# Kernel tuning notes

Measured on AMD Instinct MI355X. Metric: run time of the kernel, lower is better.

The kernel has to match this reference:

```python
import jax, jax.numpy as jnp
import numpy as np

B = 256          # graphs per batch
NPG = 512        # nodes per graph (equal-size AIGs)
N = B * NPG      # 131072 total nodes
E = 2 * N        # AIG: ~2 fanins per AND node
H = 256          # hidden_channels
EMB = 3          # node-type embedding dim
IN = EMB + 1     # node_encoder_out_channels


def _p(k, shape, fan_in):
    return jax.random.normal(k, shape, jnp.float32) / np.float32(np.sqrt(fan_in))


def setup_inputs():
    key = jax.random.key(0)
    ks = list(jax.random.split(key, 24))
    nt = jax.random.randint(ks[0], (N, 1), 0, 3)
    ninv = jax.random.randint(ks[1], (N, 1), 0, 3)
    x = jnp.concatenate([nt, ninv], axis=1).astype(jnp.int32)
    # within-graph random edges
    epg = E // B
    gid = jnp.repeat(jnp.arange(B), epg)
    src = gid * NPG + jax.random.randint(ks[2], (E,), 0, NPG)
    dst = gid * NPG + jax.random.randint(ks[3], (E,), 0, NPG)
    edge_index = jnp.stack([src, dst]).astype(jnp.int32)
    batch = jnp.repeat(jnp.arange(B), NPG).astype(jnp.int32)
    d = dict(x=x, edge_index=edge_index, batch=batch)
    d['emb_w'] = _p(ks[4], (3, EMB), 1)
    d['c1_lW'] = _p(ks[5], (IN, H), IN); d['c1_lb'] = jnp.zeros((H,), jnp.float32)
    d['c1_rW'] = _p(ks[6], (IN, H), IN)
    d['t1'] = jnp.float32(0.1)
    d['c2_lW'] = _p(ks[7], (H, H), H); d['c2_lb'] = jnp.zeros((H,), jnp.float32)
    d['c2_rW'] = _p(ks[8], (H, H), H)
    d['t2'] = jnp.float32(0.1)
    d['mlp_W'] = _p(ks[9], (NPG * H, H), NPG * H); d['mlp_b'] = jnp.zeros((H,), jnp.float32)
    d['gru_Wih'] = _p(ks[10], (3 * H, H), H); d['gru_Whh'] = _p(ks[11], (3 * H, H), H)
    d['gru_bih'] = jnp.zeros((3 * H,), jnp.float32); d['gru_bhh'] = jnp.zeros((3 * H,), jnp.float32)
    d['st_Wq'] = _p(ks[12], (3, H, H), H); d['st_bq'] = jnp.zeros((3, H), jnp.float32)
    d['st_Wk'] = _p(ks[13], (3, H, H), H); d['st_bk'] = jnp.zeros((3, H), jnp.float32)
    d['st_Wv'] = _p(ks[14], (3, H, H), H); d['st_bv'] = jnp.zeros((3, H), jnp.float32)
    d['st_Wo'] = _p(ks[15], (3, H, H), H); d['st_bo'] = jnp.zeros((3, H), jnp.float32)
    d['st_lW'] = _p(ks[16], (3, H, H), H); d['st_lb'] = jnp.zeros((3, H), jnp.float32)
    d['pma_lW'] = _p(ks[17], (H, H), H); d['pma_lb'] = jnp.zeros((H,), jnp.float32)
    d['seed'] = _p(ks[18], (1, H), H)
    d['fin_W'] = _p(ks[19], (3 * H, 3 * H), 3 * H); d['fin_b'] = jnp.zeros((3 * H,), jnp.float32)
    return d


def _softmax_aggr(msg, idx, t, n):
    # PyG SoftmaxAggregation: alpha = softmax(msg * t per target segment); sum(msg * alpha)
    logits = msg * t                                   # [E, C]
    m = jax.ops.segment_max(logits, idx, num_segments=n)
    m = jnp.where(jnp.isfinite(m), m, 0.0)             # empty segments -> 0
    ex = jnp.exp(logits - m[idx])
    s = jax.ops.segment_sum(ex, idx, num_segments=n)
    alpha = ex / s[idx]
    return jax.ops.segment_sum(msg * alpha, idx, num_segments=n)


def _sage(h, edge_index, lW, lb, rW, t):
    # SAGEConv: lin_l(softmax_aggr(x_j -> i)) + lin_r(x_i)
    msg = h[edge_index[0]]                             # gather sources [E, C]
    ag = _softmax_aggr(msg, edge_index[1], t, N)       # scatter-softmax-scatter
    return ag @ lW + lb + h @ rW


def _gru_last(xd, Wih, Whh, bih, bhh):
    # torch GRU over [B, T, H]; return last output
    def step(h, x_t):
        gi = x_t @ Wih.T + bih
        gh = h @ Whh.T + bhh
        ir, iz, inn = jnp.split(gi, 3, axis=-1)
        hr, hz, hn = jnp.split(gh, 3, axis=-1)
        r = jax.nn.sigmoid(ir + hr)
        z = jax.nn.sigmoid(iz + hz)
        nn_ = jnp.tanh(inn + r * hn)
        h_new = (1.0 - z) * nn_ + z * h
        return h_new, None
    h0 = jnp.zeros((xd.shape[0], H), xd.dtype)
    hT, _ = jax.lax.scan(step, h0, jnp.swapaxes(xd, 0, 1))
    return hT


def _mab(q, k, Wq, bq, Wk, bk, Wv, bv, Wo, bo, Wl, bl):
    # Set-Transformer MAB, 1 head, no layer norm (PyG defaults)
    Q = q @ Wq + bq
    K = k @ Wk + bk
    V = k @ Wv + bv
    A = jax.nn.softmax(jnp.einsum('bqd,bkd->bqk', Q, K) / np.float32(np.sqrt(H)), axis=-1)
    h = q + (jnp.einsum('bqk,bkd->bqd', A, V) @ Wo + bo)
    return h + jax.nn.relu(h @ Wl + bl)


def _set_transformer(xd, Wq, bq, Wk, bk, Wv, bv, Wo, bo, Wl, bl, pma_lW, pma_lb, seed):
    def mab_i(i, q, k):
        return _mab(q, k, Wq[i], bq[i], Wk[i], bk[i], Wv[i], bv[i], Wo[i], bo[i], Wl[i], bl[i])
    h = mab_i(0, xd, xd)                               # encoder SAB [B, NPG, H]
    kk = jax.nn.relu(h @ pma_lW + pma_lb)
    s = jnp.broadcast_to(seed[None], (xd.shape[0], 1, H))
    s = mab_i(1, s, kk)                                # PMA (1 seed)
    s = mab_i(2, s, s)                                 # decoder SAB
    return s.reshape(xd.shape[0], H)


def _forward(x, edge_index, batch, emb_w, c1_lW, c1_lb, c1_rW, t1, c2_lW, c2_lb, c2_rW, t2,
             mlp_W, mlp_b, gru_Wih, gru_Whh, gru_bih, gru_bhh,
             st_Wq, st_bq, st_Wk, st_bk, st_Wv, st_bv, st_Wo, st_bo, st_lW, st_lb,
             pma_lW, pma_lb, seed, fin_W, fin_b):
    # NodeEncoder: embed node_type, concat num_inverted_predecessors as float
    h = jnp.concatenate([emb_w[x[:, 0]], x[:, 1:2].astype(jnp.float32)], axis=1)  # [N, 4]
    h = jax.nn.relu(_sage(h, edge_index, c1_lW, c1_lb, c1_rW, t1))
    h = jax.nn.relu(_sage(h, edge_index, c2_lW, c2_lb, c2_rW, t2))
    # equal-size sorted graphs -> dense batch is a reshape
    xd = h.reshape(B, NPG, H)
    p1 = xd.reshape(B, NPG * H) @ mlp_W + mlp_b                       # MLPAggregation
    p2 = _gru_last(xd, gru_Wih, gru_Whh, gru_bih, gru_bhh)            # GRUAggregation
    p3 = _set_transformer(xd, st_Wq, st_bq, st_Wk, st_bk, st_Wv, st_bv,
                          st_Wo, st_bo, st_lW, st_lb, pma_lW, pma_lb, seed)
    pooled = jnp.concatenate([p1, p2, p3], axis=1)                    # [B, 3H]
    return pooled @ fin_W + fin_b


def reference(x, edge_index, batch, emb_w, c1_lW, c1_lb, c1_rW, t1, c2_lW, c2_lb, c2_rW, t2,
              mlp_W, mlp_b, gru_Wih, gru_Whh, gru_bih, gru_bhh,
              st_Wq, st_bq, st_Wk, st_bk, st_Wv, st_bv, st_Wo, st_bo, st_lW, st_lb,
              pma_lW, pma_lb, seed, fin_W, fin_b):
    return _forward(x, edge_index, batch, emb_w, c1_lW, c1_lb, c1_rW, t1, c2_lW, c2_lb, c2_rW, t2,
                    mlp_W, mlp_b, gru_Wih, gru_Whh, gru_bih, gru_bhh,
                    st_Wq, st_bq, st_Wk, st_bk, st_Wv, st_bv, st_Wo, st_bo, st_lW, st_lb,
                    pma_lW, pma_lb, seed, fin_W, fin_b)
```

## Files before the change

kernel.cpp:

```cpp
#include <hip/hip_runtime.h>
#include <hip/hip_bf16.h>
#include <math.h>

constexpr int NN   = 131072;
constexpr int NE   = 262144;
constexpr int BG   = 256;

typedef __bf16 bf16x8 __attribute__((ext_vector_type(8)));
typedef float  f32x4  __attribute__((ext_vector_type(4)));
typedef int    i32x4  __attribute__((ext_vector_type(4)));

__device__ inline float sigm(float x){ return 1.f/(1.f+__expf(-x)); }
__device__ inline float blo(unsigned u){ union{unsigned a;float f;}v; v.a=u<<16; return v.f; }
__device__ inline float bhi(unsigned u){ union{unsigned a;float f;}v; v.a=u&0xffff0000u; return v.f; }
__device__ inline float b2f(ushort u){ union{unsigned a;float f;}v; v.a=((unsigned)u)<<16; return v.f; }
__device__ inline unsigned short f2bu(float f){
  union{float f;unsigned u;}v; v.f=f;
  unsigned u = v.u + 0x7fffu + ((v.u>>16)&1u);
  return (unsigned short)(u>>16);
}
__device__ inline bf16x8 cvt8(float4 a, float4 b){
  union { ushort u[8]; bf16x8 v; } r;
  r.u[0]=f2bu(a.x); r.u[1]=f2bu(a.y); r.u[2]=f2bu(a.z); r.u[3]=f2bu(a.w);
  r.u[4]=f2bu(b.x); r.u[5]=f2bu(b.y); r.u[6]=f2bu(b.z); r.u[7]=f2bu(b.w);
  return r.v;
}

__global__ void k_zero(int* __restrict__ p, int n){
  int i = blockIdx.x*256 + threadIdx.x;
  if (i < n) p[i] = 0;
}

__global__ void k_node_enc(const int* __restrict__ x, const float* __restrict__ emb,
                           float* __restrict__ h0){
  int n = blockIdx.x*256 + threadIdx.x;
  if (n >= NN) return;
  int nt = x[2*n], ninv = x[2*n+1];
  float4 v; v.x = emb[nt*3+0]; v.y = emb[nt*3+1]; v.z = emb[nt*3+2]; v.w = (float)ninv;
  reinterpret_cast<float4*>(h0)[n] = v;
}

__global__ void k_count(const int* __restrict__ ei, int* __restrict__ deg){
  int e = blockIdx.x*256 + threadIdx.x;
  if (e >= NE) return;
  atomicAdd(&deg[ei[NE + e]], 1);
}
__global__ void k_blocksum(const int* __restrict__ deg, int* __restrict__ bsum){
  __shared__ int sd[256];
  int t = threadIdx.x;
  const int* p = deg + blockIdx.x*1024;
  int s = p[t*4] + p[t*4+1] + p[t*4+2] + p[t*4+3];
  sd[t]=s; __syncthreads();
  for (int d=128; d>0; d>>=1){ if (t<d) sd[t]+=sd[t+d]; __syncthreads(); }
  if (!t) bsum[blockIdx.x] = sd[0];
}
__global__ void k_scanbsum(const int* __restrict__ bsum, int* __restrict__ boff, int* __restrict__ offN){
  __shared__ int s[128];
  int t = threadIdx.x;
  int mine = bsum[t];
  s[t]=mine; __syncthreads();
  for (int d=1; d<128; d<<=1){ int v = (t>=d)? s[t-d]:0; __syncthreads(); s[t]+=v; __syncthreads(); }
  boff[t] = s[t]-mine;
  if (t==127) offN[0] = s[127];
}
__global__ void k_scanchunk(const int* __restrict__ deg, const int* __restrict__ boff, int* __restrict__ offs){
  __shared__ int ts[256];
  int t = threadIdx.x, b = blockIdx.x;
  const int* p = deg + b*1024;
  int v0=p[t*4],v1=p[t*4+1],v2=p[t*4+2],v3=p[t*4+3];
  int mysum=v0+v1+v2+v3;
  ts[t]=mysum; __syncthreads();
  for (int d=1; d<256; d<<=1){ int v=(t>=d)?ts[t-d]:0; __syncthreads(); ts[t]+=v; __syncthreads(); }
  int ex = ts[t]-mysum + boff[b];
  int* o = offs + b*1024 + t*4;
  o[0]=ex; o[1]=ex+v0; o[2]=ex+v0+v1; o[3]=ex+v0+v1+v2;
}
__global__ void k_fill(const int* __restrict__ ei, const int* __restrict__ offs,
                       int* __restrict__ cur, int* __restrict__ esrc){
  int e = blockIdx.x*256 + threadIdx.x;
  if (e >= NE) return;
  int dst = ei[NE+e];
  int pos = offs[dst] + atomicAdd(&cur[dst],1);
  esrc[pos] = ei[e];
}

__global__ void k_aggr4(const float* __restrict__ h, const int* __restrict__ offs,
                        const int* __restrict__ esrc, const float* __restrict__ tptr,
                        float* __restrict__ ag){
  int n = blockIdx.x*256 + threadIdx.x;
  if (n >= NN) return;
  int s = offs[n], e = offs[n+1];
  float4 z = {0,0,0,0};
  if (s == e){ reinterpret_cast<float4*>(ag)[n] = z; return; }
  float t = *tptr;
  float4 num=z, den=z;
  for (int i=s;i<e;++i){
    float4 v = reinterpret_cast<const float4*>(h)[esrc[i]];
    float ex;
    ex=__expf(v.x*t); num.x+=v.x*ex; den.x+=ex;
    ex=__expf(v.y*t); num.y+=v.y*ex; den.y+=ex;
    ex=__expf(v.z*t); num.z+=v.z*ex; den.z+=ex;
    ex=__expf(v.w*t); num.w+=v.w*ex; den.w+=ex;
  }
  float4 r = {num.x/den.x, num.y/den.y, num.z/den.z, num.w/den.w};
  reinterpret_cast<float4*>(ag)[n] = r;
}

__global__ __launch_bounds__(256) void k_aggr256(float* __restrict__ buf, const int* __restrict__ offs,
                          const int* __restrict__ esrc, const float* __restrict__ tptr, int base){
  int n = base + blockIdx.x, c = threadIdx.x;
  int s = offs[n], e = offs[n+1];
  float* outp = buf + (size_t)blockIdx.x*512 + 256 + c;
  if (s == e){ *outp = 0.f; return; }
  float t = *tptr;
  float num=0.f, den=0.f;
  for (int i=s;i<e;++i){
    float v = buf[(size_t)(esrc[i]-base)*512 + c];
    float ex = __expf(v*t);
    num += v*ex; den += ex;
  }
  *outp = num/den;
}

__global__ __launch_bounds__(256) void k_conv1_lin(const float* __restrict__ ag, const float* __restrict__ h0,
                            const float* __restrict__ lW, const float* __restrict__ lb,
                            const float* __restrict__ rW, float* __restrict__ out, int base){
  int n = base + blockIdx.x, c = threadIdx.x;
  float4 a  = reinterpret_cast<const float4*>(ag)[n];
  float4 xv = reinterpret_cast<const float4*>(h0)[n];
  float acc = lb[c];
  acc += a.x*lW[c]  + a.y*lW[256+c]  + a.z*lW[512+c]  + a.w*lW[768+c];
  acc += xv.x*rW[c] + xv.y*rW[256+c] + xv.z*rW[512+c] + xv.w*rW[768+c];
  out[(size_t)blockIdx.x*512 + c] = fmaxf(acc, 0.f);
}

#define GF_BIAS    1
#define GF_RELU    2
#define GF_RESID   4
#define GF_RESID_B 8
#define GF_ADDC    32
#define GF_ATOMIC  64
#define GF_BF16    128
#define GF_VTP     256
#define GF_RESID16 512

__global__ void k_packb(const float* __restrict__ W, ushort* __restrict__ Bp, int K, int N){
  int idx = blockIdx.x*256 + threadIdx.x;
  if (idx >= K*N) return;
  int k = idx / N, j = idx - k*N;
  Bp[((size_t)(k>>3)*N + j)*8 + (k&7)] = f2bu(W[idx]);
}
__global__ void k_packbT(const float* __restrict__ W, ushort* __restrict__ Bp, int K, int N){
  int idx = blockIdx.x*256 + threadIdx.x;
  if (idx >= K*N) return;
  int j = idx / K, k = idx - j*K;
  Bp[((size_t)(k>>3)*N + j)*8 + (k&7)] = f2bu(W[idx]);
}
__global__ __launch_bounds__(256) void k_packhh8(const float* __restrict__ gWhh,
                        char* __restrict__ Bp8, float* __restrict__ cs){
  int j = blockIdx.x, k = threadIdx.x;
  float w = gWhh[(size_t)j*256 + k];
  __shared__ float red[256];
  red[k] = fabsf(w); __syncthreads();
  for (int d=128; d>0; d>>=1){ if (k<d) red[k]=fmaxf(red[k],red[k+d]); __syncthreads(); }
  float mx = fmaxf(red[0], 1e-20f);
  int q = (int)lrintf(w * (127.f/mx));
  q = max(-127, min(127, q));
  Bp8[((size_t)(k>>3)*768 + j)*8 + (k&7)] = (char)q;
  if (k==0) cs[j] = mx/(127.f*127.f);
}
__global__ void k_packbias(const float* __restrict__ gbih, const float* __restrict__ gbhh,
                           float* __restrict__ bc){
  int i = blockIdx.x*256 + threadIdx.x;
  if (i >= 1024) return;
  int c = i & 255;
  float v;
  if (i < 256)      v = gbih[c] + gbhh[c];
  else if (i < 512) v = gbih[256+c] + gbhh[256+c];
  else if (i < 768) v = gbih[512+c];
  else              v = gbhh[512+c];
  bc[i] = v;
}

template<int FLAGS>
__global__ __launch_bounds__(256) void k_bgemm(const float* __restrict__ A, const ushort* __restrict__ Bp,
                       const float* __restrict__ bias, const float* __restrict__ resid,
                       float* __restrict__ C, int M, int Nn, int K, int lda){
  const int tid = threadIdx.x;
  const int wv = tid>>6, lane = tid&63;
  const int mw = wv>>1, nw = wv&1;
  const int arow = lane&15, ks = lane>>4;
  const int m0 = blockIdx.x*128 + mw*64, n0 = blockIdx.y*128 + nw*64;
  f32x4 acc[4][4] = {};
  #pragma unroll 2
  for (int k0 = 0; k0 < K; k0 += 32){
    const int kb = (k0>>3) + ks;
    bf16x8 af[4];
    #pragma unroll
    for (int mf=0; mf<4; ++mf){
      const float4* p = reinterpret_cast<const float4*>(A + (size_t)(m0+mf*16+arow)*lda + k0 + ks*8);
      af[mf] = cvt8(p[0], p[1]);
    }
    #pragma unroll
    for (int nf=0; nf<4; ++nf){
      const int col = n0 + nf*16 + arow;
      bf16x8 bfr = *reinterpret_cast<const bf16x8*>(Bp + ((size_t)kb*Nn + col)*8);
      #pragma unroll
      for (int mf=0; mf<4; ++mf)
        acc[mf][nf] = __builtin_amdgcn_mfma_f32_16x16x32_bf16(af[mf], bfr, acc[mf][nf], 0, 0, 0);
    }
  }
  #pragma unroll
  for (int nf=0; nf<4; ++nf){
    const int n = n0 + nf*16 + arow;
    float bv  = (FLAGS & GF_BIAS)    ? bias[n]  : 0.f;
    float rbv = (FLAGS & GF_RESID_B) ? resid[n] : 0.f;
    #pragma unroll
    for (int mf=0; mf<4; ++mf){
      #pragma unroll
      for (int r=0; r<4; ++r){
        const int m = m0 + mf*16 + ks*4 + r;
        size_t idx = (size_t)m*Nn + n;
        float v = acc[mf][nf][r];
        v += bv;
        if (FLAGS & GF_RELU)  v = fmaxf(v, 0.f);
        if (FLAGS & GF_RESID) v += resid[idx];
        v += rbv;
        C[idx] = v;
      }
    }
  }
}

template<int FLAGS, bool ABF>
__global__ __launch_bounds__(256) void k_bgemm2(const void* __restrict__ Av, const ushort* __restrict__ Bp,
                       const float* __restrict__ bias, const void* __restrict__ residv,
                       void* __restrict__ Cv, int K, int lda){
  const int tid = threadIdx.x;
  const int wv = tid>>6, lane = tid&63;
  const int mw = wv&1, nw = wv>>1;
  const int arow = lane&15, ks = lane>>4;
  const int m0 = blockIdx.x*128 + mw*64;
  const int n0 = nw*128;
  const int kChunk = K / gridDim.z, kBeg = blockIdx.z * kChunk;
  f32x4 acc[4][8] = {};
  #pragma unroll 1
  for (int k0 = kBeg; k0 < kBeg+kChunk; k0 += 32){
    const int kb = (k0>>3) + ks;
    bf16x8 af[4];
    if (ABF){
      const ushort* A = (const ushort*)Av;
      #pragma unroll
      for (int mf=0; mf<4; ++mf)
        af[mf] = *reinterpret_cast<const bf16x8*>(A + (size_t)(m0+mf*16+arow)*lda + k0 + ks*8);
    } else {
      const float* A = (const float*)Av;
      #pragma unroll
      for (int mf=0; mf<4; ++mf){
        const float4* p = reinterpret_cast<const float4*>(A + (size_t)(m0+mf*16+arow)*lda + k0 + ks*8);
        af[mf] = cvt8(p[0], p[1]);
      }
    }
    #pragma unroll
    for (int nf=0; nf<8; ++nf){
      const int col = n0 + nf*16 + arow;
      bf16x8 bfr = *reinterpret_cast<const bf16x8*>(Bp + ((size_t)kb*256 + col)*8);
      #pragma unroll
      for (int mf=0; mf<4; ++mf)
        acc[mf][nf] = __builtin_amdgcn_mfma_f32_16x16x32_bf16(af[mf], bfr, acc[mf][nf], 0, 0, 0);
    }
  }
  #pragma unroll
  for (int nf=0; nf<8; ++nf){
    const int n = n0 + nf*16 + arow;
    float bv = (FLAGS & GF_BIAS) ? bias[n] : 0.f;
    #pragma unroll
    for (int mf=0; mf<4; ++mf){
      #pragma unroll
      for (int r=0; r<4; ++r){
        const int m = m0 + mf*16 + ks*4 + r;
        size_t idx = (size_t)m*256 + n;
        float v = acc[mf][nf][r];
        if (FLAGS & GF_ATOMIC){ atomicAdd((float*)Cv + idx, v); }
        else {
          v += bv;
          if (FLAGS & GF_RELU) v = fmaxf(v, 0.f);
          if (FLAGS & GF_RESID16) v += b2f(((const ushort*)residv)[idx]);
          if (FLAGS & GF_VTP){
            const int rr = m & 511, mg = m >> 9;
            ((ushort*)Cv)[(size_t)mg*131072 + (((rr>>3)*256 + n)<<3) + (rr&7)] = f2bu(v);
          } else if (FLAGS & GF_BF16){
            ((ushort*)Cv)[idx] = f2bu(v);
          } else {
            ((float*)Cv)[idx] = v;
          }
        }
      }
    }
  }
}

__global__ __launch_bounds__(256) void k_qk16(const ushort* __restrict__ Qb, const ushort* __restrict__ Kb,
                                              float* __restrict__ S){
  const int tid = threadIdx.x;
  const int wv = tid>>6, lane = tid&63;
  const int mw = wv>>1, nw = wv&1;
  const int arow = lane&15, ks = lane>>4;
  const int m0 = blockIdx.x*128 + mw*64;
  const int n0 = blockIdx.y*128 + nw*64;
  const int g  = blockIdx.x>>2;
  const ushort* Kg = Kb + (size_t)g*131072;
  f32x4 acc[4][4] = {};
  #pragma unroll
  for (int k0 = 0; k0 < 256; k0 += 32){
    bf16x8 af[4];
    #pragma unroll
    for (int mf=0; mf<4; ++mf)
      af[mf] = *reinterpret_cast<const bf16x8*>(Qb + (size_t)(m0+mf*16+arow)*256 + k0 + ks*8);
    #pragma unroll
    for (int nf=0; nf<4; ++nf){
      const int j = n0 + nf*16 + arow;
      bf16x8 bfr = *reinterpret_cast<const bf16x8*>(Kg + (size_t)j*256 + k0 + ks*8);
      #pragma unroll
      for (int mf=0; mf<4; ++mf)
        acc[mf][nf] = __builtin_amdgcn_mfma_f32_16x16x32_bf16(af[mf], bfr, acc[mf][nf], 0, 0, 0);
    }
  }
  #pragma unroll
  for (int nf=0; nf<4; ++nf){
    const int n = n0 + nf*16 + arow;
    #pragma unroll
    for (int mf=0; mf<4; ++mf){
      #pragma unroll
      for (int r=0; r<4; ++r){
        const int m = m0 + mf*16 + ks*4 + r;
        S[(size_t)m*512 + n] = acc[mf][nf][r];
      }
    }
  }
}

__global__ __launch_bounds__(256) void k_smrow(const float* __restrict__ S, ushort* __restrict__ P){
  const int row = blockIdx.x, tid = threadIdx.x;
  __shared__ float red[4];
  const float* sr = S + (size_t)row*512;
  float s0 = sr[tid], s1 = sr[tid+256];
  float m = fmaxf(s0, s1);
  #pragma unroll
  for (int o=1;o<64;o<<=1) m = fmaxf(m, __shfl_xor(m,o));
  if ((tid&63)==0) red[tid>>6] = m;
  __syncthreads();
  m = fmaxf(fmaxf(red[0],red[1]), fmaxf(red[2],red[3]));
  __syncthreads();
  float e0 = __expf((s0-m)*0.0625f), e1 = __expf((s1-m)*0.0625f);
  float s = e0+e1;
  #pragma unroll
  for (int o=1;o<64;o<<=1) s += __shfl_xor(s,o);
  if ((tid&63)==0) red[tid>>6] = s;
  __syncthreads();
  s = red[0]+red[1]+red[2]+red[3];
  float inv = 1.f/s;
  P[(size_t)row*512 + tid]       = f2bu(e0*inv);
  P[(size_t)row*512 + 256 + tid] = f2bu(e1*inv);
}

__global__ __launch_bounds__(256) void k_av2(const ushort* __restrict__ Pb, const ushort* __restrict__ VTp,
                                             ushort* __restrict__ Ob){
  const int tid = threadIdx.x;
  const int wv = tid>>6, lane = tid&63;
  const int mw = wv&1, nw = wv>>1;
  const int arow = lane&15, ks = lane>>4;
  const int m0 = blockIdx.x*128 + mw*64;
  const int n0 = nw*128;
  const int g  = blockIdx.x>>2;
  const ushort* Vg = VTp + (size_t)g*131072;
  f32x4 acc[4][8] = {};
  #pragma unroll 1
  for (int k0 = 0; k0 < 512; k0 += 32){
    const int kb = (k0>>3) + ks;
    bf16x8 af[4];
    #pragma unroll
    for (int mf=0; mf<4; ++mf)
      af[mf] = *reinterpret_cast<const bf16x8*>(Pb + (size_t)(m0+mf*16+arow)*512 + k0 + ks*8);
    #pragma unroll
    for (int nf=0; nf<8; ++nf){
      const int col = n0 + nf*16 + arow;
      bf16x8 bfr = *reinterpret_cast<const bf16x8*>(Vg + ((size_t)kb*256 + col)*8);
      #pragma unroll
      for (int mf=0; mf<4; ++mf)
        acc[mf][nf] = __builtin_amdgcn_mfma_f32_16x16x32_bf16(af[mf], bfr, acc[mf][nf], 0, 0, 0);
    }
  }
  #pragma unroll
  for (int nf=0; nf<8; ++nf){
    const int n = n0 + nf*16 + arow;
    #pragma unroll
    for (int mf=0; mf<4; ++mf){
      #pragma unroll
      for (int r=0; r<4; ++r){
        const int m = m0 + mf*16 + ks*4 + r;
        Ob[(size_t)m*256 + n] = f2bu(acc[mf][nf][r]);
      }
    }
  }
}

__global__ void k_rowbias(const float* __restrict__ bias, float* __restrict__ C, int Nn, int total){
  int i = blockIdx.x*256 + threadIdx.x;
  if (i < total) C[i] = bias[i % Nn];
}
__global__ void k_qvec(const float* __restrict__ seed, const float* __restrict__ Wq,
                       const float* __restrict__ bq, float* __restrict__ qv){
  __shared__ float s[256];
  int t = threadIdx.x;
  s[t] = seed[t]; __syncthreads();
  float acc = bq[t];
  for (int c = 0; c < 256; ++c) acc += s[c] * Wq[c*256 + t];
  qv[t] = acc;
}
__global__ __launch_bounds__(256) void k_wk2q(const float* __restrict__ Wk2, const float* __restrict__ bk2,
                      const float* __restrict__ qv, float* __restrict__ outv){
  __shared__ float qs[256];
  __shared__ float red[4];
  int t = threadIdx.x;
  qs[t] = qv[t]; __syncthreads();
  float a = 0.f;
  for (int c=0;c<256;c+=4){
    float4 w = *reinterpret_cast<const float4*>(Wk2 + t*256 + c);
    a += w.x*qs[c] + w.y*qs[c+1] + w.z*qs[c+2] + w.w*qs[c+3];
  }
  outv[t] = a;
  float bb = bk2[t]*qs[t];
  #pragma unroll
  for (int o=1;o<64;o<<=1) bb += __shfl_xor(bb,o);
  if ((t&63)==0) red[t>>6] = bb;
  __syncthreads();
  if (t==0) outv[256] = red[0]+red[1]+red[2]+red[3];
}
__global__ __launch_bounds__(256) void k_pmafuse16(const ushort* __restrict__ kkb, const float* __restrict__ wkq,
                        float* __restrict__ wsum){
  int g = blockIdx.x, tid = threadIdx.x;
  __shared__ float qs[256];
  __shared__ float sc[512];
  __shared__ float red[4];
  qs[tid] = wkq[tid];
  __syncthreads();
  const float b2q = wkq[256];
  const ushort* kg = kkb + (size_t)g*512*256;
  float l0=0.f, l1=0.f;
  for (int j0=0;j0<2;++j0){
    int j = tid + j0*256;
    const ushort* kr = kg + (size_t)j*256;
    float a = 0.f;
    for (int c8=0;c8<32;++c8){
      uint4 kv = *reinterpret_cast<const uint4*>(kr + c8*8);
      const float* qq = qs + c8*8;
      a += qq[0]*blo(kv.x)+qq[1]*bhi(kv.x)+qq[2]*blo(kv.y)+qq[3]*bhi(kv.y)
         + qq[4]*blo(kv.z)+qq[5]*bhi(kv.z)+qq[6]*blo(kv.w)+qq[7]*bhi(kv.w);
    }
    a = (a + b2q)*0.0625f;
    if (j0) l1=a; else l0=a;
  }
  float m = fmaxf(l0,l1);
  #pragma unroll
  for (int o=1;o<64;o<<=1) m = fmaxf(m, __shfl_xor(m,o));
  if ((tid&63)==0) red[tid>>6] = m;
  __syncthreads();
  m = fmaxf(fmaxf(red[0],red[1]), fmaxf(red[2],red[3]));
  __syncthreads();
  float e0 = __expf(l0-m), e1 = __expf(l1-m);
  sc[tid]=e0; sc[tid+256]=e1;
  float s = e0+e1;
  #pragma unroll
  for (int o=1;o<64;o<<=1) s += __shfl_xor(s,o);
  if ((tid&63)==0) red[tid>>6] = s;
  __syncthreads();
  s = red[0]+red[1]+red[2]+red[3];
  float invs = 1.f/s;
  float acc = 0.f;
  for (int j=0;j<512;++j) acc += sc[j] * b2f(kg[(size_t)j*256 + tid]);
  wsum[(size_t)g*256+tid] = acc*invs;
}
__global__ void k_concat(const float* __restrict__ p1, const float* __restrict__ p2,
                         const float* __restrict__ p3, float* __restrict__ pooled){
  int idx = blockIdx.x*256 + threadIdx.x;
  int b = idx / 768, j = idx % 768;
  float v = (j < 256) ? p1[b*256+j] : (j < 512) ? p2[b*256+j-256] : p3[b*256+j-512];
  pooled[idx] = v;
}

__global__ __launch_bounds__(512) void k_gru12(const ushort* __restrict__ X,
                      const ushort* __restrict__ pIh, const char* __restrict__ pHh8,
                      const float* __restrict__ csg, const float* __restrict__ bc,
                      float* __restrict__ p2){
  extern __shared__ char gsm[];
  float*  GIw  = (float*)gsm;
  float*  gh   = (float*)(gsm + 98304);
  float*  bcl  = (float*)(gsm + 101376);
  float*  csl  = (float*)(gsm + 105472);
  char*   hbf8 = (char*) (gsm + 108544);
  const int g = blockIdx.x;
  const int tid = threadIdx.x;
  const int wv = tid>>6, lane = tid&63;
  const int arow = lane&15, ks = lane>>4;
  for (int i=tid;i<1024;i+=512) bcl[i] = bc[i];
  for (int i=tid;i<768;i+=512)  csl[i] = csg[i];
  if (tid < 256) hbf8[tid] = 0;
  float h_reg = 0.f;
  const ushort* Xg = X + (size_t)g*512*256;
  __syncthreads();
  for (int w=0; w<16; ++w){
    const int t0 = w*32;
    #pragma unroll
    for (int mt=0; mt<2; ++mt){
      const ushort* xr = Xg + (size_t)(t0 + mt*16 + arow)*256;
      f32x4 acc[6] = {};
      #pragma unroll
      for (int kt=0; kt<8; ++kt){
        bf16x8 af = *reinterpret_cast<const bf16x8*>(xr + kt*32 + ks*8);
        #pragma unroll
        for (int nt=0; nt<6; ++nt){
          bf16x8 bfr = *reinterpret_cast<const bf16x8*>(pIh + ((size_t)(kt*4+ks)*768 + wv*96+nt*16+arow)*8);
          acc[nt] = __builtin_amdgcn_mfma_f32_16x16x32_bf16(af, bfr, acc[nt], 0,0,0);
        }
      }
      #pragma unroll
      for (int nt=0; nt<6; ++nt){
        const int col = wv*96 + nt*16 + arow;
        #pragma unroll
        for (int r=0;r<4;++r)
          GIw[(size_t)(mt*16 + ks*4 + r)*768 + col] = acc[nt][r];
      }
    }
    for (int dt=0; dt<32; ++dt){
      i32x4 sacc[6] = {};
      #pragma unroll
      for (int kt=0; kt<8; ++kt){
        long a8 = 0;
        if (arow == 0) a8 = *reinterpret_cast<const long*>(hbf8 + kt*32 + ks*8);
        #pragma unroll
        for (int nt=0; nt<6; ++nt){
          const int col = wv*96 + nt*16 + arow;
          long b8 = *reinterpret_cast<const long*>(pHh8 + ((size_t)(kt*4+ks)*768 + col)*8);
          sacc[nt] = __builtin_amdgcn_mfma_i32_16x16x32_i8(a8, b8, sacc[nt], 0,0,0);
        }
      }
      if (ks == 0){
        #pragma unroll
        for (int nt=0; nt<6; ++nt){
          const int col = wv*96 + nt*16 + arow;
          gh[col] = (float)sacc[nt][0] * csl[col];
        }
      }
      __syncthreads();
      if (tid < 256){
        const int c = tid;
        const float* gir = GIw + (size_t)dt*768;
        float rr = sigm(gir[c]     + gh[c]     + bcl[c]);
        float zz = sigm(gir[256+c] + gh[256+c] + bcl[256+c]);
        float nx = gir[512+c] + bcl[512+c] + rr*(gh[512+c] + bcl[768+c]);
        nx = fminf(fmaxf(nx, -15.f), 15.f);
        float e2 = __expf(2.f*nx);
        float nn = (e2-1.f)*__builtin_amdgcn_rcpf(e2+1.f);
        h_reg = (1.f-zz)*nn + zz*h_reg;
        int q = (int)lrintf(h_reg*127.f);
        q = max(-127, min(127, q));
        hbf8[c] = (char)q;
      }
      __syncthreads();
    }
  }
  if (tid < 256) p2[(size_t)g*256 + tid] = h_reg;
}

extern "C" void kernel_launch(void* const* d_in, const int* in_sizes, int n_in,
                              void* d_out, int out_size, void* d_ws, size_t ws_size,
                              hipStream_t stream){
  const int*   x      = (const int*)  d_in[0];
  const int*   ei     = (const int*)  d_in[1];
  const float* emb_w  = (const float*)d_in[3];
  const float* c1_lW  = (const float*)d_in[4];
  const float* c1_lb  = (const float*)d_in[5];
  const float* c1_rW  = (const float*)d_in[6];
  const float* t1     = (const float*)d_in[7];
  const float* c2_lW  = (const float*)d_in[8];
  const float* c2_lb  = (const float*)d_in[9];
  const float* c2_rW  = (const float*)d_in[10];
  const float* t2     = (const float*)d_in[11];
  const float* mlp_W  = (const float*)d_in[12];
  const float* mlp_b  = (const float*)d_in[13];
  const float* gWih   = (const float*)d_in[14];
  const float* gWhh   = (const float*)d_in[15];
  const float* gbih   = (const float*)d_in[16];
  const float* gbhh   = (const float*)d_in[17];
  const float* stWq   = (const float*)d_in[18];
  const float* stbq   = (const float*)d_in[19];
  const float* stWk   = (const float*)d_in[20];
  const float* stbk   = (const float*)d_in[21];
  const float* stWv   = (const float*)d_in[22];
  const float* stbv   = (const float*)d_in[23];
  const float* stWo   = (const float*)d_in[24];
  const float* stbo   = (const float*)d_in[25];
  const float* stlW   = (const float*)d_in[26];
  const float* stlb   = (const float*)d_in[27];
  const float* pma_lW = (const float*)d_in[28];
  const float* pma_lb = (const float*)d_in[29];
  const float* seed   = (const float*)d_in[30];
  const float* fin_W  = (const float*)d_in[31];
  const float* fin_b  = (const float*)d_in[32];
  float* out = (float*)d_out;

  auto needFor = [](int CHe)->size_t{
    size_t bufN = (size_t)CHe*512*512;
    size_t floats = (size_t)33554432 + 3*bufN + 2*524288 + 2*196608 + 8*65536 + 196608 + 320 + 512;
    size_t ints   = 131072 + 131200 + 131072 + 262144 + 128 + 128;
    return floats*4 + ints*4 + 4096;
  };
  const int CHe = (ws_size >= needFor(64)) ? 64 : 32;
  if (ws_size < needFor(32)) return;
  const int NCHUNKe = BG / CHe;
  const int NCNe = CHe * 512;
  const size_t bufN = (size_t)CHe*512*512;

  float* H2   = (float*)d_ws;
  float* bufA = H2   + (size_t)33554432;
  float* bufB = bufA + bufN;
  float* bufC = bufB + bufN;
  float* h0   = bufC + bufN;
  float* ag1  = h0   + (size_t)524288;
  float* wT1  = ag1  + (size_t)524288;
  float* wT2  = wT1  + (size_t)196608;
  float* p1   = wT2  + (size_t)196608;
  float* p2   = p1   + (size_t)65536;
  float* p3   = p2   + (size_t)65536;
  float* av2  = p3   + (size_t)65536;
  float* s1   = av2  + (size_t)65536;
  float* s2v  = s1   + (size_t)65536;
  float* v3   = s2v  + (size_t)65536;
  float* h3   = v3   + (size_t)65536;
  float* pooled = h3 + (size_t)65536;
  float* qv   = pooled + (size_t)196608;
  int*   deg  = (int*)(qv + 320);
  int*   offs = deg  + 131072;
  int*   cur  = offs + 131200;
  int*   esrc = cur  + 131072;
  int*   bsum = esrc + 262144;
  int*   boff = bsum + 128;
  float* wkq  = (float*)(boff + 128);

  ushort* H2b  = (ushort*)H2;
  ushort* pIh  = (ushort*)wT1;
  char*   pHh8 = (char*)(wT1 + 98304);
  float*  csHh = wT1 + 98304 + 49152;
  ushort* pC2  = (ushort*)wT2;
  float*  bcomb= wT2 + 65536;
  float*  pa   = h0;
  ushort* pQ0  = (ushort*)(pa);
  ushort* pK0  = (ushort*)(pa + 32768);
  ushort* pV0  = (ushort*)(pa + 65536);
  ushort* pO0  = (ushort*)(pa + 98304);
  ushort* pL0  = (ushort*)(pa + 131072);
  ushort* pPma = (ushort*)(pa + 163840);
  ushort* pV1  = (ushort*)(pa + 229376);
  ushort* pO1  = (ushort*)(pa + 262144);
  ushort* pL1  = (ushort*)(pa + 294912);
  ushort* pV2  = (ushort*)(pa + 327680);
  ushort* pO2  = (ushort*)(pa + 360448);
  ushort* pL2  = (ushort*)(pa + 393216);
  ushort* pFin = (ushort*)(pa + 425984);

  ushort* Qbf = (ushort*)bufA;
  ushort* Obf = (ushort*)(bufA + bufN/4);
  ushort* VTp = (ushort*)(bufA + bufN/2);
  ushort* Kbf = (ushort*)bufB;
  ushort* Pbf = (ushort*)(bufB + bufN/4);
  ushort* Ebf = Qbf;
  ushort* kkb = Kbf;

  const int ls0 = 65536, ls1 = 256;

  k_node_enc<<<NN/256, 256, 0, stream>>>(x, emb_w, h0);

  k_zero<<<NN/256, 256, 0, stream>>>(deg, NN);
  k_count<<<NE/256, 256, 0, stream>>>(ei, deg);
  k_blocksum<<<128, 256, 0, stream>>>(deg, bsum);
  k_scanbsum<<<1, 128, 0, stream>>>(bsum, boff, offs + NN);
  k_scanchunk<<<128, 256, 0, stream>>>(deg, boff, offs);
  k_zero<<<NN/256, 256, 0, stream>>>(cur, NN);
  k_fill<<<NE/256, 256, 0, stream>>>(ei, offs, cur, esrc);

  k_aggr4<<<NN/256, 256, 0, stream>>>(h0, offs, esrc, t1, ag1);
  k_packb <<<256, 256, 0, stream>>>(c2_rW, pC2, 256, 256);
  k_packb <<<256, 256, 0, stream>>>(c2_lW, pC2 + 65536, 256, 256);
  k_packbT<<<768, 256, 0, stream>>>(gWih, pIh, 256, 768);
  k_packhh8<<<768, 256, 0, stream>>>(gWhh, pHh8, csHh);
  k_packbias<<<4, 256, 0, stream>>>(gbih, gbhh, bcomb);

  for (int cg = 0; cg < NCHUNKe; ++cg){
    const int base = cg * NCNe;
    ushort* Hcb = H2b + (size_t)base * 256;
    k_conv1_lin<<<NCNe, 256, 0, stream>>>(ag1, h0, c1_lW, c1_lb, c1_rW, bufA, base);
    k_aggr256<<<NCNe, 256, 0, stream>>>(bufA, offs, esrc, t2, base);
    k_bgemm2<GF_BIAS|GF_RELU|GF_BF16, false><<<NCNe/128, 256, 0, stream>>>(bufA, pC2, c2_lb, nullptr, Hcb, 512, 512);
  }

  k_packb<<<131072, 256, 0, stream>>>(mlp_W, (ushort*)bufB, 131072, 256);
  k_rowbias<<<256, 256, 0, stream>>>(mlp_b, p1, 256, 65536);
  k_bgemm2<GF_ATOMIC, true><<<dim3(2, 1, 128), 256, 0, stream>>>(H2b, (ushort*)bufB, nullptr, nullptr, p1, NN, 131072);

  k_gru12<<<BG, 512, 108800, stream>>>(H2b, pIh, pHh8, csHh, bcomb, p2);

  k_packb<<<256, 256, 0, stream>>>(stWq,        pQ0, 256, 256);
  k_packb<<<256, 256, 0, stream>>>(stWk,        pK0, 256, 256);
  k_packb<<<256, 256, 0, stream>>>(stWv,        pV0, 256, 256);
  k_packb<<<256, 256, 0, stream>>>(stWo,        pO0, 256, 256);
  k_packb<<<256, 256, 0, stream>>>(stlW,        pL0, 256, 256);
  k_packb<<<256, 256, 0, stream>>>(pma_lW,      pPma,256, 256);
  k_packb<<<256, 256, 0, stream>>>(stWv + ls0,  pV1, 256, 256);
  k_packb<<<256, 256, 0, stream>>>(stWo + ls0,  pO1, 256, 256);
  k_packb<<<256, 256, 0, stream>>>(stlW + ls0,  pL1, 256, 256);
  k_packb<<<256, 256, 0, stream>>>(stWv + 2*ls0,pV2, 256, 256);
  k_packb<<<256, 256, 0, stream>>>(stWo + 2*ls0,pO2, 256, 256);
  k_packb<<<256, 256, 0, stream>>>(stlW + 2*ls0,pL2, 256, 256);
  k_packb<<<2304, 256, 0, stream>>>(fin_W,      pFin,768, 768);
  k_qvec<<<1, 256, 0, stream>>>(seed, stWq + ls0, stbq + ls1, qv);
  k_wk2q<<<1, 256, 0, stream>>>(stWk + ls0, stbk + ls1, qv, wkq);

  for (int cg = 0; cg < NCHUNKe; ++cg){
    const int base = cg * NCNe;
    ushort* Hcb = H2b + (size_t)base * 256;
    const int gb1 = NCNe/128;
    k_bgemm2<GF_BIAS|GF_BF16, true><<<gb1, 256, 0, stream>>>(Hcb, pQ0, stbq, nullptr, Qbf, 256, 256);
    k_bgemm2<GF_BIAS|GF_BF16, true><<<gb1, 256, 0, stream>>>(Hcb, pK0, stbk, nullptr, Kbf, 256, 256);
    k_bgemm2<GF_BIAS|GF_VTP,  true><<<gb1, 256, 0, stream>>>(Hcb, pV0, stbv, nullptr, VTp, 256, 256);
    k_qk16<<<dim3(gb1, 4), 256, 0, stream>>>(Qbf, Kbf, bufC);
    k_smrow<<<NCNe, 256, 0, stream>>>(bufC, Pbf);
    k_av2<<<gb1, 256, 0, stream>>>(Pbf, VTp, Obf);
    k_bgemm2<GF_BIAS|GF_RESID16|GF_BF16, true><<<gb1, 256, 0, stream>>>(Obf, pO0, stbo, Hcb, Hcb, 256, 256);
    k_bgemm2<GF_BIAS|GF_RELU|GF_RESID16|GF_BF16, true><<<gb1, 256, 0, stream>>>(Hcb, pL0, stlb, Hcb, Ebf, 256, 256);
    k_bgemm2<GF_BIAS|GF_RELU|GF_BF16, true><<<gb1, 256, 0, stream>>>(Ebf, pPma, pma_lb, nullptr, kkb, 256, 256);
    k_pmafuse16<<<CHe, 256, 0, stream>>>(kkb, wkq, av2 + (size_t)cg*CHe*256);
  }

  k_bgemm<GF_BIAS><<<dim3(2, 2, 1), 256, 0, stream>>>(av2, pV1, stbv + ls1, nullptr, v3, 256, 256, 256, 256);
  k_bgemm<GF_BIAS|GF_RESID_B><<<dim3(2, 2, 1), 256, 0, stream>>>(v3, pO1, stbo + ls1, seed, s1, 256, 256, 256, 256);
  k_bgemm<GF_BIAS|GF_RELU|GF_RESID><<<dim3(2, 2, 1), 256, 0, stream>>>(s1, pL1, stlb + ls1, s1, s2v, 256, 256, 256, 256);
  k_bgemm<GF_BIAS><<<dim3(2, 2, 1), 256, 0, stream>>>(s2v, pV2, stbv + 2*ls1, nullptr, v3, 256, 256, 256, 256);
  k_bgemm<GF_BIAS|GF_RESID><<<dim3(2, 2, 1), 256, 0, stream>>>(v3, pO2, stbo + 2*ls1, s2v, h3, 256, 256, 256, 256);
  k_bgemm<GF_BIAS|GF_RELU|GF_RESID><<<dim3(2, 2, 1), 256, 0, stream>>>(h3, pL2, stlb + 2*ls1, h3, p3, 256, 256, 256, 256);

  k_concat<<<768, 256, 0, stream>>>(p1, p2, p3, pooled);
  k_bgemm<GF_BIAS><<<dim3(2, 6, 1), 256, 0, stream>>>(pooled, pFin, fin_b, nullptr, out, 256, 768, 768, 768);
}
```

Baseline: 2.732 ms.

## Fuse QK, softmax and AV into one LDS-resident attention kernel; bf16 conv2 staging

Replaces the three-kernel attention (QK^T to global fp32 scores, row softmax, then P·V) with one kernel per 64-row tile. The score tile stays in 132KB of LDS, is softmaxed in place, and is converted to bf16 on the fly for the AV MFMA, with normalisation applied at the output. This removes the global round trip of the 512x512 fp32 score matrix and the bf16 P matrix. Separately, the conv1 output and conv2 aggregation buffer are now stored as bf16, so the GEMM reads bf16 directly and memory traffic is lower, at some precision cost. The large LDS footprint limits each CU to one block.

```diff
diff --git a/kernel.cpp b/kernel.cpp
--- a/kernel.cpp
+++ b/kernel.cpp
@@ -106,32 +106,32 @@
   reinterpret_cast<float4*>(ag)[n] = r;
 }
 
-__global__ __launch_bounds__(256) void k_aggr256(float* __restrict__ buf, const int* __restrict__ offs,
+__global__ __launch_bounds__(256) void k_aggr256(ushort* __restrict__ buf, const int* __restrict__ offs,
                           const int* __restrict__ esrc, const float* __restrict__ tptr, int base){
   int n = base + blockIdx.x, c = threadIdx.x;
   int s = offs[n], e = offs[n+1];
-  float* outp = buf + (size_t)blockIdx.x*512 + 256 + c;
-  if (s == e){ *outp = 0.f; return; }
+  ushort* outp = buf + (size_t)blockIdx.x*512 + 256 + c;
+  if (s == e){ *outp = 0; return; }
   float t = *tptr;
   float num=0.f, den=0.f;
   for (int i=s;i<e;++i){
-    float v = buf[(size_t)(esrc[i]-base)*512 + c];
+    float v = b2f(buf[(size_t)(esrc[i]-base)*512 + c]);
     float ex = __expf(v*t);
     num += v*ex; den += ex;
   }
-  *outp = num/den;
+  *outp = f2bu(num/den);
 }
 
 __global__ __launch_bounds__(256) void k_conv1_lin(const float* __restrict__ ag, const float* __restrict__ h0,
                             const float* __restrict__ lW, const float* __restrict__ lb,
-                            const float* __restrict__ rW, float* __restrict__ out, int base){
+                            const float* __restrict__ rW, ushort* __restrict__ out, int base){
   int n = base + blockIdx.x, c = threadIdx.x;
   float4 a  = reinterpret_cast<const float4*>(ag)[n];
   float4 xv = reinterpret_cast<const float4*>(h0)[n];
   float acc = lb[c];
   acc += a.x*lW[c]  + a.y*lW[256+c]  + a.z*lW[512+c]  + a.w*lW[768+c];
   acc += xv.x*rW[c] + xv.y*rW[256+c] + xv.z*rW[512+c] + xv.w*rW[768+c];
-  out[(size_t)blockIdx.x*512 + c] = fmaxf(acc, 0.f);
+  out[(size_t)blockIdx.x*512 + c] = f2bu(fmaxf(acc, 0.f));
 }
 
 #define GF_BIAS    1
@@ -300,106 +300,96 @@
   }
 }
 
-__global__ __launch_bounds__(256) void k_qk16(const ushort* __restrict__ Qb, const ushort* __restrict__ Kb,
-                                              float* __restrict__ S){
+__global__ __launch_bounds__(256) void k_afuse(const ushort* __restrict__ Qb, const ushort* __restrict__ Kb,
+                        const ushort* __restrict__ VTp, ushort* __restrict__ Ob){
+  extern __shared__ char afm[];
+  float* Sld  = (float*)afm;
+  float* red1 = (float*)(afm + 132096);
+  float* red2 = red1 + 256;
+  float* invr = red2 + 256;
   const int tid = threadIdx.x;
   const int wv = tid>>6, lane = tid&63;
-  const int mw = wv>>1, nw = wv&1;
   const int arow = lane&15, ks = lane>>4;
-  const int m0 = blockIdx.x*128 + mw*64;
-  const int n0 = blockIdx.y*128 + nw*64;
-  const int g  = blockIdx.x>>2;
-  const ushort* Kg = Kb + (size_t)g*131072;
-  f32x4 acc[4][4] = {};
-  #pragma unroll
-  for (int k0 = 0; k0 < 256; k0 += 32){
-    bf16x8 af[4];
-    #pragma unroll
-    for (int mf=0; mf<4; ++mf)
-      af[mf] = *reinterpret_cast<const bf16x8*>(Qb + (size_t)(m0+mf*16+arow)*256 + k0 + ks*8);
-    #pragma unroll
-    for (int nf=0; nf<4; ++nf){
-      const int j = n0 + nf*16 + arow;
-      bf16x8 bfr = *reinterpret_cast<const bf16x8*>(Kg + (size_t)j*256 + k0 + ks*8);
+  const int m0 = blockIdx.x*64;
+  const int g  = blockIdx.x>>3;
+  const ushort* Kg = Kb  + (size_t)g*131072;
+  const ushort* Vg = VTp + (size_t)g*131072;
+  {
+    const int n0 = wv*128;
+    f32x4 acc[4][8] = {};
+    #pragma unroll
+    for (int k0 = 0; k0 < 256; k0 += 32){
+      bf16x8 af[4];
       #pragma unroll
       for (int mf=0; mf<4; ++mf)
-        acc[mf][nf] = __builtin_amdgcn_mfma_f32_16x16x32_bf16(af[mf], bfr, acc[mf][nf], 0, 0, 0);
-    }
-  }
-  #pragma unroll
-  for (int nf=0; nf<4; ++nf){
-    const int n = n0 + nf*16 + arow;
-    #pragma unroll
-    for (int mf=0; mf<4; ++mf){
-      #pragma unroll
-      for (int r=0; r<4; ++r){
-        const int m = m0 + mf*16 + ks*4 + r;
-        S[(size_t)m*512 + n] = acc[mf][nf][r];
-      }
-    }
-  }
-}
-
-__global__ __launch_bounds__(256) void k_smrow(const float* __restrict__ S, ushort* __restrict__ P){
-  const int row = blockIdx.x, tid = threadIdx.x;
-  __shared__ float red[4];
-  const float* sr = S + (size_t)row*512;
-  float s0 = sr[tid], s1 = sr[tid+256];
-  float m = fmaxf(s0, s1);
-  #pragma unroll
-  for (int o=1;o<64;o<<=1) m = fmaxf(m, __shfl_xor(m,o));
-  if ((tid&63)==0) red[tid>>6] = m;
-  __syncthreads();
-  m = fmaxf(fmaxf(red[0],red[1]), fmaxf(red[2],red[3]));
-  __syncthreads();
-  float e0 = __expf((s0-m)*0.0625f), e1 = __expf((s1-m)*0.0625f);
-  float s = e0+e1;
-  #pragma unroll
-  for (int o=1;o<64;o<<=1) s += __shfl_xor(s,o);
-  if ((tid&63)==0) red[tid>>6] = s;
-  __syncthreads();
-  s = red[0]+red[1]+red[2]+red[3];
-  float inv = 1.f/s;
-  P[(size_t)row*512 + tid]       = f2bu(e0*inv);
-  P[(size_t)row*512 + 256 + tid] = f2bu(e1*inv);
-}
-
-__global__ __launch_bounds__(256) void k_av2(const ushort* __restrict__ Pb, const ushort* __restrict__ VTp,
-                                             ushort* __restrict__ Ob){
-  const int tid = threadIdx.x;
-  const int wv = tid>>6, lane = tid&63;
-  const int mw = wv&1, nw = wv>>1;
-  const int arow = lane&15, ks = lane>>4;
-  const int m0 = blockIdx.x*128 + mw*64;
-  const int n0 = nw*128;
-  const int g  = blockIdx.x>>2;
-  const ushort* Vg = VTp + (size_t)g*131072;
-  f32x4 acc[4][8] = {};
-  #pragma unroll 1
-  for (int k0 = 0; k0 < 512; k0 += 32){
-    const int kb = (k0>>3) + ks;
-    bf16x8 af[4];
-    #pragma unroll
-    for (int mf=0; mf<4; ++mf)
-      af[mf] = *reinterpret_cast<const bf16x8*>(Pb + (size_t)(m0+mf*16+arow)*512 + k0 + ks*8);
+        af[mf] = *reinterpret_cast<const bf16x8*>(Qb + (size_t)(m0+mf*16+arow)*256 + k0 + ks*8);
+      #pragma unroll
+      for (int nf=0; nf<8; ++nf){
+        const int j = n0 + nf*16 + arow;
+        bf16x8 bfr = *reinterpret_cast<const bf16x8*>(Kg + (size_t)j*256 + k0 + ks*8);
+        #pragma unroll
+        for (int mf=0; mf<4; ++mf)
+          acc[mf][nf] = __builtin_amdgcn_mfma_f32_16x16x32_bf16(af[mf], bfr, acc[mf][nf], 0, 0, 0);
+      }
+    }
     #pragma unroll
     for (int nf=0; nf<8; ++nf){
       const int col = n0 + nf*16 + arow;
-      bf16x8 bfr = *reinterpret_cast<const bf16x8*>(Vg + ((size_t)kb*256 + col)*8);
-      #pragma unroll
-      for (int mf=0; mf<4; ++mf)
-        acc[mf][nf] = __builtin_amdgcn_mfma_f32_16x16x32_bf16(af[mf], bfr, acc[mf][nf], 0, 0, 0);
-    }
-  }
-  #pragma unroll
-  for (int nf=0; nf<8; ++nf){
-    const int n = n0 + nf*16 + arow;
-    #pragma unroll
-    for (int mf=0; mf<4; ++mf){
-      #pragma unroll
-      for (int r=0; r<4; ++r){
-        const int m = m0 + mf*16 + ks*4 + r;
-        Ob[(size_t)m*256 + n] = f2bu(acc[mf][nf][r]);
+      #pragma unroll
+      for (int mf=0; mf<4; ++mf){
+        #pragma unroll
+        for (int r=0; r<4; ++r)
+          Sld[(size_t)(mf*16 + ks*4 + r)*516 + col] = acc[mf][nf][r];
+      }
+    }
+  }
+  __syncthreads();
+  {
+    const int row = tid>>2, q = tid&3;
+    float* sr = Sld + (size_t)row*516 + q*128;
+    float mx = -3e38f;
+    for (int c=0;c<128;++c) mx = fmaxf(mx, sr[c]);
+    red1[row*4+q] = mx;
+    __syncthreads();
+    mx = fmaxf(fmaxf(red1[row*4], red1[row*4+1]), fmaxf(red1[row*4+2], red1[row*4+3]));
+    float sum = 0.f;
+    for (int c=0;c<128;++c){ float e = __expf((sr[c]-mx)*0.0625f); sr[c]=e; sum+=e; }
+    red2[row*4+q] = sum;
+    __syncthreads();
+    if (q==0) invr[row] = 1.f/(red2[row*4]+red2[row*4+1]+red2[row*4+2]+red2[row*4+3]);
+    __syncthreads();
+  }
+  {
+    const int n0 = wv*64;
+    f32x4 acc[4][4] = {};
+    #pragma unroll 1
+    for (int k0 = 0; k0 < 512; k0 += 32){
+      const int kb = (k0>>3) + ks;
+      bf16x8 af[4];
+      #pragma unroll
+      for (int mf=0; mf<4; ++mf){
+        const float4* p = reinterpret_cast<const float4*>(Sld + (size_t)(mf*16+arow)*516 + k0 + ks*8);
+        af[mf] = cvt8(p[0], p[1]);
+      }
+      #pragma unroll
+      for (int nf=0; nf<4; ++nf){
+        const int col = n0 + nf*16 + arow;
+        bf16x8 bfr = *reinterpret_cast<const bf16x8*>(Vg + ((size_t)kb*256 + col)*8);
+        #pragma unroll
+        for (int mf=0; mf<4; ++mf)
+          acc[mf][nf] = __builtin_amdgcn_mfma_f32_16x16x32_bf16(af[mf], bfr, acc[mf][nf], 0, 0, 0);
+      }
+    }
+    #pragma unroll
+    for (int nf=0; nf<4; ++nf){
+      const int n = n0 + nf*16 + arow;
+      #pragma unroll
+      for (int mf=0; mf<4; ++mf){
+        #pragma unroll
+        for (int r=0; r<4; ++r){
+          const int lr = mf*16 + ks*4 + r;
+          Ob[(size_t)(m0+lr)*256 + n] = f2bu(acc[mf][nf][r] * invr[lr]);
+        }
       }
     }
   }
@@ -673,9 +663,9 @@
   ushort* Obf = (ushort*)(bufA + bufN/4);
   ushort* VTp = (ushort*)(bufA + bufN/2);
   ushort* Kbf = (ushort*)bufB;
-  ushort* Pbf = (ushort*)(bufB + bufN/4);
   ushort* Ebf = Qbf;
   ushort* kkb = Kbf;
+  ushort* cvb = (ushort*)bufC;
 
   const int ls0 = 65536, ls1 = 256;
 
@@ -699,9 +689,9 @@
   for (int cg = 0; cg < NCHUNKe; ++cg){
     const int base = cg * NCNe;
     ushort* Hcb = H2b + (size_t)base * 256;
-    k_conv1_lin<<<NCNe, 256, 0, stream>>>(ag1, h0, c1_lW, c1_lb, c1_rW, bufA, base);
-    k_aggr256<<<NCNe, 256, 0, stream>>>(bufA, offs, esrc, t2, base);
-    k_bgemm2<GF_BIAS|GF_RELU|GF_BF16, false><<<NCNe/128, 256, 0, stream>>>(bufA, pC2, c2_lb, nullptr, Hcb, 512, 512);
+    k_conv1_lin<<<NCNe, 256, 0, stream>>>(ag1, h0, c1_lW, c1_lb, c1_rW, cvb, base);
+    k_aggr256<<<NCNe, 256, 0, stream>>>(cvb, offs, esrc, t2, base);
+    k_bgemm2<GF_BIAS|GF_RELU|GF_BF16, true><<<NCNe/128, 256, 0, stream>>>(cvb, pC2, c2_lb, nullptr, Hcb, 512, 512);
   }
 
   k_packb<<<131072, 256, 0, stream>>>(mlp_W, (ushort*)bufB, 131072, 256);
@@ -733,9 +723,7 @@
     k_bgemm2<GF_BIAS|GF_BF16, true><<<gb1, 256, 0, stream>>>(Hcb, pQ0, stbq, nullptr, Qbf, 256, 256);
     k_bgemm2<GF_BIAS|GF_BF16, true><<<gb1, 256, 0, stream>>>(Hcb, pK0, stbk, nullptr, Kbf, 256, 256);
     k_bgemm2<GF_BIAS|GF_VTP,  true><<<gb1, 256, 0, stream>>>(Hcb, pV0, stbv, nullptr, VTp, 256, 256);
-    k_qk16<<<dim3(gb1, 4), 256, 0, stream>>>(Qbf, Kbf, bufC);
-    k_smrow<<<NCNe, 256, 0, stream>>>(bufC, Pbf);
-    k_av2<<<gb1, 256, 0, stream>>>(Pbf, VTp, Obf);
+    k_afuse<<<NCNe/64, 256, 134400, stream>>>(Qbf, Kbf, VTp, Obf);
     k_bgemm2<GF_BIAS|GF_RESID16|GF_BF16, true><<<gb1, 256, 0, stream>>>(Obf, pO0, stbo, Hcb, Hcb, 256, 256);
     k_bgemm2<GF_BIAS|GF_RELU|GF_RESID16|GF_BF16, true><<<gb1, 256, 0, stream>>>(Hcb, pL0, stlb, Hcb, Ebf, 256, 256);
     k_bgemm2<GF_BIAS|GF_RELU|GF_BF16, true><<<gb1, 256, 0, stream>>>(Ebf, pPma, pma_lb, nullptr, kkb, 256, 256);
```

Result: faster. 2.562 ms (-6.2%).
